# Kernel tuning notes

Measured on AMD Instinct MI355X. Metric: run time of the kernel, lower is better.

## Reference

```python
import jax, jax.numpy as jnp
import numpy as np

EMBED_DIM = 1024
NUM_HEADS = 16
HEAD_DIM = EMBED_DIM // NUM_HEADS
WINDOW_SIZE = 256
BATCH = 2
SEQ = 2048


def setup_inputs() -> dict:
    key = jax.random.key(0)
    ks = jax.random.split(key, 5)
    s = 1.0 / np.sqrt(EMBED_DIM)
    return {
        "x": jax.random.normal(ks[0], (BATCH, SEQ, EMBED_DIM), dtype=jnp.float32),
        "Wq": jax.random.normal(ks[1], (EMBED_DIM, EMBED_DIM), dtype=jnp.float32) * s,
        "Wk": jax.random.normal(ks[2], (EMBED_DIM, EMBED_DIM), dtype=jnp.float32) * s,
        "Wv": jax.random.normal(ks[3], (EMBED_DIM, EMBED_DIM), dtype=jnp.float32) * s,
        "Wo": jax.random.normal(ks[4], (EMBED_DIM, EMBED_DIM), dtype=jnp.float32) * s,
    }


def _split_heads(t):
    # [B, S, E] -> [B, H, S, D]
    b, s, _ = t.shape
    return t.reshape(b, s, NUM_HEADS, HEAD_DIM).transpose(0, 2, 1, 3)


def reference(x, Wq, Wk, Wv, Wo):
    b, s, _ = x.shape
    # nn.Linear(bias=False): y = x @ W.T
    q = _split_heads(x @ Wq.T)
    k = _split_heads(x @ Wk.T)
    v = _split_heads(x @ Wv.T)
    scores = jnp.einsum("bhqd,bhkd->bhqk", q, k) / np.sqrt(HEAD_DIM).astype(np.float32)
    i = jnp.arange(s)[:, None]
    j = jnp.arange(s)[None, :]
    # causal sliding window: attend to j in [i - window_size + 1, i]
    allowed = (j <= i) & (j >= i - WINDOW_SIZE + 1)
    scores = jnp.where(allowed[None, None], scores, -jnp.inf)
    probs = jax.nn.softmax(scores, axis=-1)
    ctx = jnp.einsum("bhqk,bhkd->bhqd", probs, v)  # [B,H,S,D]
    ctx = ctx.transpose(0, 2, 1, 3).reshape(b, s, EMBED_DIM)
    return ctx @ Wo.T
```

## Files before the change

### kernel.cpp

```cpp
#include <hip/hip_runtime.h>
#include <hip/hip_bf16.h>
#include <stdint.h>


#define EDIM 1024
#define NH 16
#define HD 64
#define WIN 256
#define BB 2
#define SS 2048
#define MR (BB*SS)
#define NQKV 3072

typedef __attribute__((ext_vector_type(8))) short short8;
typedef __attribute__((ext_vector_type(4))) short short4v;
typedef __attribute__((ext_vector_type(4))) float f32x4;

__device__ __forceinline__ unsigned short f2bf(float f) {
  union { float f; uint32_t u; } c; c.f = f;
  uint32_t r = (c.u + 0x7FFFu + ((c.u >> 16) & 1u)) >> 16;
  return (unsigned short)r;
}

__device__ __forceinline__ unsigned pack_bf2(float a, float b) {
  return (unsigned)f2bf(a) | ((unsigned)f2bf(b) << 16);
}

template<int N> __device__ __forceinline__ void wait_vm_lgkm0() {
  if constexpr (N == 3) asm volatile("s_waitcnt vmcnt(3) lgkmcnt(0)" ::: "memory");
  else if constexpr (N == 4) asm volatile("s_waitcnt vmcnt(4) lgkmcnt(0)" ::: "memory");
  else if constexpr (N == 6) asm volatile("s_waitcnt vmcnt(6) lgkmcnt(0)" ::: "memory");
  else asm volatile("s_waitcnt vmcnt(0) lgkmcnt(0)" ::: "memory");
}

__global__ __launch_bounds__(256) void cvt_all(const float* __restrict__ x,
                                               const float* __restrict__ Wq,
                                               const float* __restrict__ Wk,
                                               const float* __restrict__ Wv,
                                               const float* __restrict__ Wo,
                                               unsigned short* __restrict__ dst) {
  const int i = blockIdx.x * 256 + threadIdx.x;
  const float* s; int off;
  if (i < 524288) { s = x; off = i; }
  else {
    const int j = i - 524288, wsel = j >> 17;
    off = j & 131071;
    s = wsel == 0 ? Wq : wsel == 1 ? Wk : wsel == 2 ? Wv : Wo;
  }
  const float4* s4 = (const float4*)s;
  float4 a = s4[2*off], b = s4[2*off+1];
  short8 o;
  o[0]=(short)f2bf(a.x); o[1]=(short)f2bf(a.y); o[2]=(short)f2bf(a.z); o[3]=(short)f2bf(a.w);
  o[4]=(short)f2bf(b.x); o[5]=(short)f2bf(b.y); o[6]=(short)f2bf(b.z); o[7]=(short)f2bf(b.w);
  ((short8*)dst)[i] = o;
}

template<typename OutT, int BM, int BN, int WM, int WN>
__global__ __launch_bounds__(WM*WN*64) void gemm_ring(const unsigned short* __restrict__ A,
                                                      const unsigned short* __restrict__ Bw,
                                                      OutT* __restrict__ C,
                                                      int M, int N, int K, int nbx) {
  constexpr int NT = WM * WN * 64;
  constexpr int MI = BM / (WM * 16);
  constexpr int NI = BN / (WN * 16);
  constexpr int LA = (BM * 4) / NT;
  constexpr int LB = (BN * 4) / NT;
  constexpr int LT = LA + LB;
  constexpr int TPB = (BM + BN) * 64;
  __shared__ __align__(16) char smem[3 * TPB];
  const int t = threadIdx.x, lane = t & 63;
  const int w = t >> 6, wr = w & (WM - 1), wc = w / WM;
  const int nwg = gridDim.x, bid = blockIdx.x;
  const int wg = (bid & 7) * (nwg >> 3) + (bid >> 3);
  const int m0 = (wg / nbx) * BM, n0 = (wg % nbx) * BN;
  const int KT = K >> 5;

  auto stage = [&](char* dA, char* dB, int kt) {
#pragma unroll
    for (int r = 0; r < LA; ++r) {
      const int chunk = r * NT + t;
      const int row = chunk >> 2, c = chunk & 3;
      const int sc = c ^ ((row >> 1) & 3);
      __builtin_amdgcn_global_load_lds(
        (const __attribute__((address_space(1))) char*)(A + (size_t)(m0 + row) * K + kt + sc * 8),
        (__attribute__((address_space(3))) char*)(dA + chunk * 16), 16, 0, 0);
    }
#pragma unroll
    for (int r = 0; r < LB; ++r) {
      const int chunk = r * NT + t;
      const int row = chunk >> 2, c = chunk & 3;
      const int sc = c ^ ((row >> 1) & 3);
      __builtin_amdgcn_global_load_lds(
        (const __attribute__((address_space(1))) char*)(Bw + (size_t)(n0 + row) * K + kt + sc * 8),
        (__attribute__((address_space(3))) char*)(dB + chunk * 16), 16, 0, 0);
    }
  };

  f32x4 acc[MI][NI] = {};
  stage(smem, smem + BM * 64, 0);
  stage(smem + TPB, smem + TPB + BM * 64, 32);
  wait_vm_lgkm0<LT>();
  __builtin_amdgcn_s_barrier();
  __builtin_amdgcn_sched_barrier(0);

  int cur = 0;
  for (int tt = 0; tt < KT; ++tt) {
    int sb = cur + 2; if (sb >= 3) sb -= 3;
    int nt2 = tt + 2; if (nt2 >= KT) nt2 -= KT;
    char* dA = smem + sb * TPB;
    stage(dA, dA + BM * 64, nt2 << 5);
    const char* rA = smem + cur * TPB;
    const char* rB = rA + BM * 64;
    short8 af[MI], bfr[NI];
    const int chq = (lane >> 4);
#pragma unroll
    for (int mi = 0; mi < MI; ++mi) {
      const int row = wr * (BM / WM) + mi * 16 + (lane & 15);
      af[mi] = *(const short8*)(rA + row * 64 + ((chq ^ ((row >> 1) & 3)) << 4));
    }
#pragma unroll
    for (int ni = 0; ni < NI; ++ni) {
      const int row = wc * (BN / WN) + ni * 16 + (lane & 15);
      bfr[ni] = *(const short8*)(rB + row * 64 + ((chq ^ ((row >> 1) & 3)) << 4));
    }
#pragma unroll
    for (int mi = 0; mi < MI; ++mi)
#pragma unroll
      for (int ni = 0; ni < NI; ++ni)
        acc[mi][ni] = __builtin_amdgcn_mfma_f32_16x16x32_bf16(af[mi], bfr[ni], acc[mi][ni], 0, 0, 0);
    wait_vm_lgkm0<LT>();
    __builtin_amdgcn_s_barrier();
    __builtin_amdgcn_sched_barrier(0);
    cur = cur + 1 == 3 ? 0 : cur + 1;
  }
#pragma unroll
  for (int mi = 0; mi < MI; ++mi) {
    const int rb = m0 + wr * (BM / WM) + mi * 16 + ((lane >> 4) << 2);
#pragma unroll
    for (int ni = 0; ni < NI; ++ni) {
      const int col = n0 + wc * (BN / WN) + ni * 16 + (lane & 15);
#pragma unroll
      for (int reg = 0; reg < 4; ++reg) {
        const float v = acc[mi][ni][reg];
        const size_t idx = (size_t)(rb + reg) * N + col;
        if constexpr (sizeof(OutT) == 2) ((unsigned short*)C)[idx] = f2bf(v);
        else ((float*)C)[idx] = v;
      }
    }
  }
}

__global__ __launch_bounds__(256) void attn_kernel(const unsigned short* __restrict__ qkv,
                                                   unsigned short* __restrict__ ctx) {
  __shared__ __align__(16) unsigned short Ks[64*64];
  __shared__ __align__(16) unsigned short VTs[64*64];
  __shared__ __align__(16) unsigned short PT[4][64*16];
  const int t = threadIdx.x, lane = t & 63, w = t >> 6;
  const int bid = blockIdx.x;
  const int swz = (bid & 7) * 128 + (bid >> 3);
  const int qt = swz & 31, bh = swz >> 5;
  const int b = bh >> 4, h = bh & 15;
  const int q0 = qt << 6;
  const int qw0 = q0 + (w << 4);
  const unsigned short* qb = qkv + (size_t)b * SS * NQKV + h * HD;
  const unsigned short* kb = qb + EDIM;
  const unsigned short* vb = qb + 2*EDIM;
  short8 aq[2];
  {
    const size_t roff = (size_t)(qw0 + (lane & 15)) * NQKV + ((lane >> 4) << 3);
    aq[0] = *(const short8*)(qb + roff);
    aq[1] = *(const short8*)(qb + roff + 32);
  }
  const unsigned vt0 = (unsigned)(uintptr_t)(__attribute__((address_space(3))) char*)((char*)VTs);
  const unsigned trbase = vt0 + ((lane & 15) << 3) + ((lane >> 4) << 7);
  const unsigned pt0 = (unsigned)(uintptr_t)(__attribute__((address_space(3))) char*)((char*)&PT[w][0]);
  const unsigned pabase0 = pt0 + ((lane >> 4) << 8) + ((lane & 15) << 3);
  char* ptw = (char*)&PT[w][0];
  const int qrelb = (w << 4) + (((lane >> 4) & 3) << 2);
  f32x4 oacc[4] = {};
  float lacc[4] = {0.f, 0.f, 0.f, 0.f};
  const int t_lo = qt >= 4 ? qt - 4 : 0;
  for (int kt = t_lo; kt <= qt; ++kt) {
    const int kv0 = kt << 6;
    __syncthreads();
#pragma unroll
    for (int r = 0; r < 2; ++r) {
      const int o = r*4096 + t*16;
      const int key = o >> 7;
      const int colb = (o & 127) ^ ((key & 7) << 4);
      __builtin_amdgcn_global_load_lds(
        (const __attribute__((address_space(1))) char*)(kb + (size_t)(kv0 + key) * NQKV + (colb >> 1)),
        (__attribute__((address_space(3))) char*)((char*)Ks + o), 16, 0, 0);
    }
#pragma unroll
    for (int i = 0; i < 2; ++i) {
      const int p8 = (w << 6) + lane + (i << 8);
      const int band = p8 >> 7, rr = p8 & 127, ordv = rr >> 3, q8 = rr & 7;
      const int k = ((ordv & 7) << 3) + ((ordv >> 3) << 2) + (q8 >> 1);
      const int d = (band << 4) + ((q8 & 1) << 3);
      __builtin_amdgcn_global_load_lds(
        (const __attribute__((address_space(1))) char*)(vb + (size_t)(kv0 + k) * NQKV + d),
        (__attribute__((address_space(3))) char*)((char*)VTs + p8*16), 16, 0, 0);
    }
    __syncthreads();
    f32x4 sc[4] = {};
    __builtin_amdgcn_s_setprio(1);
#pragma unroll
    for (int kf = 0; kf < 4; ++kf) {
#pragma unroll
      for (int c = 0; c < 2; ++c) {
        const int krow = (kf << 4) + (lane & 15);
        const int k0 = (c << 5) + ((lane >> 4) << 3);
        const int off = ((krow << 7) + (k0 << 1)) ^ ((krow & 7) << 4);
        short8 bk = *(const short8*)((const char*)Ks + off);
        sc[kf] = __builtin_amdgcn_mfma_f32_16x16x32_bf16(aq[c], bk, sc[kf], 0, 0, 0);
      }
    }
    __builtin_amdgcn_s_setprio(0);
    const bool mc = (kt == qt);
    const bool mw = (qt >= 4) && (kt == t_lo);
#pragma unroll
    for (int kf = 0; kf < 4; ++kf) {
      const int krel = (kf << 4) + (lane & 15);
      float p[4];
#pragma unroll
      for (int reg = 0; reg < 4; ++reg) {
        float e = __expf(sc[kf][reg] * 0.125f);
        if (mc | mw) {
          const bool ok = (krel <= qrelb + reg) ^ mw;
          e = ok ? e : 0.f;
        }
        p[reg] = e;
        lacc[reg] += e;
      }
      const unsigned lo = pack_bf2(p[0], p[1]);
      const unsigned hi = pack_bf2(p[2], p[3]);
      *(uint2*)(ptw + ((krel << 5) + ((lane >> 4) << 3))) = make_uint2(lo, hi);
    }
    __builtin_amdgcn_sched_barrier(0);
#pragma unroll
    for (int c2 = 0; c2 < 2; ++c2) {
      short4v plo, phi;
      const unsigned pa1 = pabase0 + (c2 << 10);
      asm volatile("ds_read_b64_tr_b16 %0, %1" : "=&v"(plo) : "v"(pa1));
      asm volatile("ds_read_b64_tr_b16 %0, %1 offset:128" : "=&v"(phi) : "v"(pa1));
      short4v lo[4], hi[4];
#pragma unroll
      for (int nf = 0; nf < 4; ++nf) {
        const unsigned a1 = trbase + (nf << 11) + (c2 << 9);
        asm volatile("ds_read_b64_tr_b16 %0, %1" : "=&v"(lo[nf]) : "v"(a1));
        asm volatile("ds_read_b64_tr_b16 %0, %1 offset:1024" : "=&v"(hi[nf]) : "v"(a1));
      }
      asm volatile("s_waitcnt lgkmcnt(0)" ::: "memory");
      __builtin_amdgcn_sched_barrier(0);
      short8 pa = __builtin_shufflevector(plo, phi, 0, 1, 2, 3, 4, 5, 6, 7);
      __builtin_amdgcn_s_setprio(1);
#pragma unroll
      for (int nf = 0; nf < 4; ++nf) {
        short8 bv = __builtin_shufflevector(lo[nf], hi[nf], 0, 1, 2, 3, 4, 5, 6, 7);
        oacc[nf] = __builtin_amdgcn_mfma_f32_16x16x32_bf16(pa, bv, oacc[nf], 0, 0, 0);
      }
      __builtin_amdgcn_s_setprio(0);
    }
  }
#pragma unroll
  for (int reg = 0; reg < 4; ++reg) {
    float l = lacc[reg];
    l += __shfl_xor(l, 1);
    l += __shfl_xor(l, 2);
    l += __shfl_xor(l, 4);
    l += __shfl_xor(l, 8);
    lacc[reg] = 1.0f / l;
  }
  unsigned short* cb = ctx + (size_t)b * SS * EDIM + h * HD;
#pragma unroll
  for (int nf = 0; nf < 4; ++nf)
#pragma unroll
    for (int reg = 0; reg < 4; ++reg) {
      const int qg = qw0 + ((lane >> 4) << 2) + reg;
      const int d = (nf << 4) + (lane & 15);
      cb[(size_t)qg * EDIM + d] = f2bf(oacc[nf][reg] * lacc[reg]);
    }
}

extern "C" void kernel_launch(void* const* d_in, const int* in_sizes, int n_in,
                              void* d_out, int out_size, void* d_ws, size_t ws_size,
                              hipStream_t stream) {
  const float* x  = (const float*)d_in[0];
  const float* Wq = (const float*)d_in[1];
  const float* Wk = (const float*)d_in[2];
  const float* Wv = (const float*)d_in[3];
  const float* Wo = (const float*)d_in[4];
  float* out = (float*)d_out;
  char* ws = (char*)d_ws;
  unsigned short* xb   = (unsigned short*)(ws);
  unsigned short* ctxb = (unsigned short*)(ws);
  unsigned short* wqkv = (unsigned short*)(ws + (size_t)(8u << 20));
  unsigned short* wob  = (unsigned short*)(ws + (size_t)(14u << 20));
  unsigned short* qkv  = (unsigned short*)(ws + (size_t)(16u << 20));

  cvt_all<<<dim3(4096), dim3(256), 0, stream>>>(x, Wq, Wk, Wv, Wo, xb);

  gemm_ring<unsigned short, 128, 128, 2, 2><<<dim3(768), dim3(256), 0, stream>>>(
      xb, wqkv, qkv, MR, NQKV, EDIM, NQKV/128);

  attn_kernel<<<dim3(1024), dim3(256), 0, stream>>>(qkv, ctxb);

  gemm_ring<float, 128, 64, 2, 2><<<dim3(512), dim3(256), 0, stream>>>(
      ctxb, wob, out, MR, EDIM, EDIM, EDIM/64);
}
```

Measured before the change: 153.0 us.

## Replace QKV projection GEMM with 256x256-tile eight-wave kernel using split-phase LDS staging

Adds a new GEMM kernel for the fused QKV projection that uses 256x256 output tiles, 8 waves per block, and double-buffered LDS filled by direct global-to-LDS loads with an XOR swizzle. Loads for the next K-tile are issued in pieces between the MFMA quarter-phases, and instruction priority is raised around the MFMA blocks. The larger tile is meant to cut global traffic per FLOP and improve MFMA utilisation. In exchange only 192 workgroups are launched, which may under-fill the GPU, and the 128 KB of LDS per block limits occupancy. The loop count of 16 is hardcoded to K=1024.

```diff
diff --git a/kernel.cpp b/kernel.cpp
--- a/kernel.cpp
+++ b/kernel.cpp
@@ -31,6 +31,12 @@
   else if constexpr (N == 4) asm volatile("s_waitcnt vmcnt(4) lgkmcnt(0)" ::: "memory");
   else if constexpr (N == 6) asm volatile("s_waitcnt vmcnt(6) lgkmcnt(0)" ::: "memory");
   else asm volatile("s_waitcnt vmcnt(0) lgkmcnt(0)" ::: "memory");
+}
+
+__device__ __forceinline__ void full_barrier() {
+  asm volatile("" ::: "memory");
+  __builtin_amdgcn_s_barrier();
+  asm volatile("" ::: "memory");
 }
 
 __global__ __launch_bounds__(256) void cvt_all(const float* __restrict__ x,
@@ -53,6 +59,133 @@
   o[0]=(short)f2bf(a.x); o[1]=(short)f2bf(a.y); o[2]=(short)f2bf(a.z); o[3]=(short)f2bf(a.w);
   o[4]=(short)f2bf(b.x); o[5]=(short)f2bf(b.y); o[6]=(short)f2bf(b.z); o[7]=(short)f2bf(b.w);
   ((short8*)dst)[i] = o;
+}
+
+__global__ __launch_bounds__(512, 2) void gemm_8w(const unsigned short* __restrict__ A,
+                                                  const unsigned short* __restrict__ Bw,
+                                                  unsigned short* __restrict__ C,
+                                                  int M, int N, int K, int nbx) {
+  __shared__ __align__(16) char smem[131072];
+  const int t = threadIdx.x, lane = t & 63;
+  const int w = t >> 6, wm = w >> 2, wn = w & 3;
+  const int nwg = gridDim.x, bid = blockIdx.x;
+  const int wg = (bid & 7) * (nwg >> 3) + (bid >> 3);
+  const int m0 = (wg / nbx) * 256, n0 = (wg % nbx) * 256;
+  const int KT = K >> 6;
+
+  auto stage_A = [&](int d, int tt, int qm_) {
+#pragma unroll
+    for (int l = 0; l < 2; ++l) {
+      const int i = l * 512 + t, r = i >> 3, c = i & 7;
+      const int row = qm_ * 64 + (r & 63) + (r >> 6) * 128;
+      __builtin_amdgcn_global_load_lds(
+        (const __attribute__((address_space(1))) char*)(A + (size_t)(m0 + row) * K + tt * 64 + ((c ^ (row & 7)) << 3)),
+        (__attribute__((address_space(3))) char*)(smem + d * 65536 + row * 128 + c * 16), 16, 0, 0);
+    }
+  };
+  auto stage_B = [&](int d, int tt, int qn_) {
+#pragma unroll
+    for (int l = 0; l < 2; ++l) {
+      const int i = l * 512 + t, r = i >> 3, c = i & 7;
+      const int row = qn_ * 32 + (r >> 5) * 64 + (r & 31);
+      __builtin_amdgcn_global_load_lds(
+        (const __attribute__((address_space(1))) char*)(Bw + (size_t)(n0 + row) * K + tt * 64 + ((c ^ (row & 7)) << 3)),
+        (__attribute__((address_space(3))) char*)(smem + d * 65536 + 32768 + row * 128 + c * 16), 16, 0, 0);
+    }
+  };
+
+  f32x4 acc[8][4] = {};
+  stage_A(0, 0, 0); stage_A(0, 0, 1); stage_B(0, 0, 0); stage_B(0, 0, 1);
+  stage_A(1, 1, 0); stage_A(1, 1, 1); stage_B(1, 1, 0); stage_B(1, 1, 1);
+
+  for (int j = 0; j < 16; ++j) {
+    const int cur = j & 1;
+    const char* rbuf = smem + cur * 65536;
+    int nt = j + 2; if (nt >= KT) nt -= KT;
+    asm volatile("s_waitcnt vmcnt(8)" ::: "memory");
+    full_barrier();
+
+    short8 af0[4][2], af1[4][2], bf0[2][2], bf1[2][2];
+#pragma unroll
+    for (int mi = 0; mi < 4; ++mi)
+#pragma unroll
+      for (int ks = 0; ks < 2; ++ks) {
+        const int row = wm * 128 + mi * 16 + (lane & 15);
+        af0[mi][ks] = *(const short8*)(rbuf + row * 128 + (((ks * 4 + (lane >> 4)) ^ (row & 7)) << 4));
+      }
+#pragma unroll
+    for (int ni = 0; ni < 2; ++ni)
+#pragma unroll
+      for (int ks = 0; ks < 2; ++ks) {
+        const int row = wn * 64 + ni * 16 + (lane & 15);
+        bf0[ni][ks] = *(const short8*)(rbuf + 32768 + row * 128 + (((ks * 4 + (lane >> 4)) ^ (row & 7)) << 4));
+      }
+    __builtin_amdgcn_s_setprio(1);
+#pragma unroll
+    for (int mi = 0; mi < 4; ++mi)
+#pragma unroll
+      for (int ni = 0; ni < 2; ++ni)
+#pragma unroll
+        for (int ks = 0; ks < 2; ++ks)
+          acc[mi][ni] = __builtin_amdgcn_mfma_f32_16x16x32_bf16(af0[mi][ks], bf0[ni][ks], acc[mi][ni], 0, 0, 0);
+    __builtin_amdgcn_s_setprio(0);
+#pragma unroll
+    for (int ni = 0; ni < 2; ++ni)
+#pragma unroll
+      for (int ks = 0; ks < 2; ++ks) {
+        const int row = wn * 64 + 32 + ni * 16 + (lane & 15);
+        bf1[ni][ks] = *(const short8*)(rbuf + 32768 + row * 128 + (((ks * 4 + (lane >> 4)) ^ (row & 7)) << 4));
+      }
+    __builtin_amdgcn_s_setprio(1);
+#pragma unroll
+    for (int mi = 0; mi < 4; ++mi)
+#pragma unroll
+      for (int ni = 0; ni < 2; ++ni)
+#pragma unroll
+        for (int ks = 0; ks < 2; ++ks)
+          acc[mi][2 + ni] = __builtin_amdgcn_mfma_f32_16x16x32_bf16(af0[mi][ks], bf1[ni][ks], acc[mi][2 + ni], 0, 0, 0);
+    __builtin_amdgcn_s_setprio(0);
+    full_barrier();
+    stage_A(cur, nt, 0); stage_B(cur, nt, 0); stage_B(cur, nt, 1);
+#pragma unroll
+    for (int mi = 0; mi < 4; ++mi)
+#pragma unroll
+      for (int ks = 0; ks < 2; ++ks) {
+        const int row = wm * 128 + 64 + mi * 16 + (lane & 15);
+        af1[mi][ks] = *(const short8*)(rbuf + row * 128 + (((ks * 4 + (lane >> 4)) ^ (row & 7)) << 4));
+      }
+    __builtin_amdgcn_s_setprio(1);
+#pragma unroll
+    for (int mi = 0; mi < 4; ++mi)
+#pragma unroll
+      for (int ni = 0; ni < 2; ++ni)
+#pragma unroll
+        for (int ks = 0; ks < 2; ++ks)
+          acc[4 + mi][2 + ni] = __builtin_amdgcn_mfma_f32_16x16x32_bf16(af1[mi][ks], bf1[ni][ks], acc[4 + mi][2 + ni], 0, 0, 0);
+    __builtin_amdgcn_s_setprio(0);
+    full_barrier();
+    stage_A(cur, nt, 1);
+    __builtin_amdgcn_s_setprio(1);
+#pragma unroll
+    for (int mi = 0; mi < 4; ++mi)
+#pragma unroll
+      for (int ni = 0; ni < 2; ++ni)
+#pragma unroll
+        for (int ks = 0; ks < 2; ++ks)
+          acc[4 + mi][ni] = __builtin_amdgcn_mfma_f32_16x16x32_bf16(af1[mi][ks], bf0[ni][ks], acc[4 + mi][ni], 0, 0, 0);
+    __builtin_amdgcn_s_setprio(0);
+  }
+#pragma unroll
+  for (int mi = 0; mi < 8; ++mi) {
+    const int rb = m0 + wm * 128 + mi * 16 + ((lane >> 4) << 2);
+#pragma unroll
+    for (int ni = 0; ni < 4; ++ni) {
+      const int col = n0 + wn * 64 + ni * 16 + (lane & 15);
+#pragma unroll
+      for (int reg = 0; reg < 4; ++reg)
+        C[(size_t)(rb + reg) * N + col] = f2bf(acc[mi][ni][reg]);
+    }
+  }
 }
 
 template<typename OutT, int BM, int BN, int WM, int WN>
@@ -301,8 +434,7 @@
 
   cvt_all<<<dim3(4096), dim3(256), 0, stream>>>(x, Wq, Wk, Wv, Wo, xb);
 
-  gemm_ring<unsigned short, 128, 128, 2, 2><<<dim3(768), dim3(256), 0, stream>>>(
-      xb, wqkv, qkv, MR, NQKV, EDIM, NQKV/128);
+  gemm_8w<<<dim3(192), dim3(512), 0, stream>>>(xb, wqkv, qkv, MR, NQKV, EDIM, NQKV/256);
 
   attn_kernel<<<dim3(1024), dim3(256), 0, stream>>>(qkv, ctxb);
 
```

Result: faster. 148.5 us (-3.0%).
